# Optimization experiments

Measured on AMD Instinct MI355X. Metric: run time of the kernel, lower is better.

The kernel has to match this reference:

```python
import jax, jax.numpy as jnp
import numpy as np

B, T, C, H = 2, 2048, 1024, 16
D = C // H  # head dim = 64


def setup_inputs() -> dict:
    key = jax.random.key(0)
    ks = jax.random.split(key, 5)
    s = 0.02
    return {
        "x": jax.random.normal(ks[0], (B, T, C), dtype=jnp.float32),
        "W_attn": jax.random.normal(ks[1], (C, 3 * C), dtype=jnp.float32) * s,
        "b_attn": jax.random.normal(ks[2], (3 * C,), dtype=jnp.float32) * s,
        "W_proj": jax.random.normal(ks[3], (C, C), dtype=jnp.float32) * s,
        "b_proj": jax.random.normal(ks[4], (C,), dtype=jnp.float32) * s,
    }


def reference(x, W_attn, b_attn, W_proj, b_proj):
    Bb, Tt, Cc = x.shape
    kqv = x @ W_attn + b_attn                     # [B,T,3C]
    q, k, v = jnp.split(kqv, 3, axis=2)           # each [B,T,C]
    # reshape to heads: [B,H,T,D]
    q = q.reshape(Bb, Tt, H, D).transpose(0, 2, 1, 3)
    k = k.reshape(Bb, Tt, H, D).transpose(0, 2, 1, 3)
    v = v.reshape(Bb, Tt, H, D).transpose(0, 2, 1, 3)
    scale = 1.0 / jnp.sqrt(jnp.float32(D))
    att = jnp.einsum('bhqd,bhkd->bhqk', q, k) * scale  # [B,H,T,T]
    causal = jnp.tril(jnp.ones((Tt, Tt), dtype=bool))
    att = jnp.where(causal[None, None], att, -jnp.inf)
    att = jax.nn.softmax(att, axis=-1)
    y = jnp.einsum('bhqk,bhkd->bhqd', att, v)      # [B,H,T,D]
    y = y.transpose(0, 2, 1, 3).reshape(Bb, Tt, Cc)
    return y @ W_proj + b_proj
```

## Files before the change

### kernel.cpp

```cpp
#include <hip/hip_runtime.h>
#include <hip/hip_bf16.h>
#include <math.h>

typedef __attribute__((ext_vector_type(4))) float f32x4;
typedef __attribute__((ext_vector_type(8))) short short8;
typedef __attribute__((ext_vector_type(4))) short short4v;

__device__ __forceinline__ short f2bf(float f) {
    union { __hip_bfloat16 h; short s; } u;
    u.h = __float2bfloat16(f);
    return u.s;
}

__device__ __forceinline__ float bf2f(short s) {
    union { float f; unsigned u; } x;
    x.u = ((unsigned)(unsigned short)s) << 16;
    return x.f;
}

__device__ __forceinline__ f32x4 mfma16(short8 a, short8 b, f32x4 c) {
    return __builtin_amdgcn_mfma_f32_16x16x32_bf16(a, b, c, 0, 0, 0);
}

__global__ __launch_bounds__(256) void cvt_bf16(const float* __restrict__ in,
                                                short* __restrict__ out, int n) {
    int i = (blockIdx.x * 256 + threadIdx.x) * 8;
    if (i >= n) return;
    float4 a = *reinterpret_cast<const float4*>(in + i);
    float4 b = *reinterpret_cast<const float4*>(in + i + 4);
    short8 o;
    o[0] = f2bf(a.x); o[1] = f2bf(a.y); o[2] = f2bf(a.z); o[3] = f2bf(a.w);
    o[4] = f2bf(b.x); o[5] = f2bf(b.y); o[6] = f2bf(b.z); o[7] = f2bf(b.w);
    *reinterpret_cast<short8*>(out + i) = o;
}

__global__ __launch_bounds__(256) void transpose_w(const float* __restrict__ W,
                                                   short* __restrict__ Wt,
                                                   int K, int N) {
    __shared__ float tile[64][68];
    const int k0 = blockIdx.x * 64;
    const int n0 = blockIdx.y * 64;
    const int tid = threadIdx.x;
    #pragma unroll
    for (int i = 0; i < 4; ++i) {
        int c = tid + i * 256;
        int r = c >> 4;
        int col4 = (c & 15) * 4;
        float4 v = *reinterpret_cast<const float4*>(W + (size_t)(k0 + r) * N + n0 + col4);
        tile[r][col4 + 0] = v.x; tile[r][col4 + 1] = v.y;
        tile[r][col4 + 2] = v.z; tile[r][col4 + 3] = v.w;
    }
    __syncthreads();
    #pragma unroll
    for (int i = 0; i < 4; ++i) {
        int c = tid + i * 256;
        int r2 = c >> 4;
        int col4 = (c & 15) * 4;
        short4v o;
        #pragma unroll
        for (int j = 0; j < 4; ++j) o[j] = f2bf(tile[col4 + j][r2]);
        *reinterpret_cast<short4v*>(Wt + (size_t)(n0 + r2) * K + k0 + col4) = o;
    }
}

template<int MODE>
__global__ __launch_bounds__(256) void gemm_bt(const short* __restrict__ A,
                                               const short* __restrict__ Bt,
                                               const float* __restrict__ bias,
                                               void* __restrict__ C,
                                               short* __restrict__ vt,
                                               int M, int N, int K) {
    constexpr int BM = 128, BN = 128, BK = 64, LDP = BK + 8;
    __shared__ short As[BM * LDP];
    __shared__ short Bs[BN * LDP];
    const int tid = threadIdx.x;
    const int lane = tid & 63, wave = tid >> 6;
    const int bm = blockIdx.x * BM, bn = blockIdx.y * BN;
    const int wr = (wave >> 1) * 64, wc = (wave & 1) * 64;
    const int g = lane >> 4, l15 = lane & 15;

    f32x4 acc[4][4] = {};

    for (int k0 = 0; k0 < K; k0 += BK) {
        __syncthreads();
        #pragma unroll
        for (int i = 0; i < 4; ++i) {
            int c = tid + i * 256;
            int r = c >> 3;
            int col = (c & 7) * 8;
            *reinterpret_cast<short8*>(&As[r * LDP + col]) =
                *reinterpret_cast<const short8*>(A + (size_t)(bm + r) * K + k0 + col);
            *reinterpret_cast<short8*>(&Bs[r * LDP + col]) =
                *reinterpret_cast<const short8*>(Bt + (size_t)(bn + r) * K + k0 + col);
        }
        __syncthreads();
        #pragma unroll
        for (int kk = 0; kk < 2; ++kk) {
            short8 af[4], bfr[4];
            #pragma unroll
            for (int m = 0; m < 4; ++m)
                af[m] = *reinterpret_cast<const short8*>(&As[(wr + m * 16 + l15) * LDP + kk * 32 + g * 8]);
            #pragma unroll
            for (int n = 0; n < 4; ++n)
                bfr[n] = *reinterpret_cast<const short8*>(&Bs[(wc + n * 16 + l15) * LDP + kk * 32 + g * 8]);
            #pragma unroll
            for (int m = 0; m < 4; ++m)
                #pragma unroll
                for (int n = 0; n < 4; ++n)
                    acc[m][n] = mfma16(af[m], bfr[n], acc[m][n]);
        }
    }

    #pragma unroll
    for (int m = 0; m < 4; ++m)
        #pragma unroll
        for (int n = 0; n < 4; ++n) {
            int gc = bn + wc + n * 16 + l15;
            float bv = bias[gc];
            int gr0 = bm + wr + m * 16 + g * 4;
            if (MODE == 0) {
                #pragma unroll
                for (int r = 0; r < 4; ++r)
                    reinterpret_cast<float*>(C)[(size_t)(gr0 + r) * N + gc] = acc[m][n][r] + bv;
            } else {
                if (gc < 2048) {
                    float sc = (gc < 1024) ? 0.125f : 1.0f;
                    short* qkp = reinterpret_cast<short*>(C);
                    #pragma unroll
                    for (int r = 0; r < 4; ++r)
                        qkp[(size_t)(gr0 + r) * 2048 + gc] = f2bf((acc[m][n][r] + bv) * sc);
                } else {
                    int cv = gc - 2048;
                    int bb = gr0 >> 11;
                    int t0 = gr0 & 2047;
                    short4v o;
                    #pragma unroll
                    for (int r = 0; r < 4; ++r) o[r] = f2bf(acc[m][n][r] + bv);
                    *reinterpret_cast<short4v*>(&vt[((size_t)(bb << 10) + cv) * 2048 + t0]) = o;
                }
            }
        }
}


template<int NMAX, int KKMAX, bool MASK>
__device__ __forceinline__ void tile_step(const short* __restrict__ Kl,
                                          const short* __restrict__ Vl,
                                          short* Ps, int l15, int g,
                                          const short8 (&qf)[2][2],
                                          f32x4 (&oacc)[2][4],
                                          f32x4 (&lacc)[2],
                                          float (&mst)[2][4],
                                          int rowbase, int colbase,
                                          short8 ones) {
    f32x4 sacc[2][NMAX + 1];
    #pragma unroll
    for (int m = 0; m < 2; ++m)
        #pragma unroll
        for (int n = 0; n <= NMAX; ++n) sacc[m][n] = f32x4{0.f, 0.f, 0.f, 0.f};
    __builtin_amdgcn_s_setprio(1);
    #pragma unroll
    for (int kk = 0; kk < 2; ++kk)
        #pragma unroll
        for (int n = 0; n <= NMAX; ++n) {
            short8 kf = *reinterpret_cast<const short8*>(Kl + (size_t)n * 16 * 2048 + kk * 32);
            sacc[0][n] = mfma16(qf[0][kk], kf, sacc[0][n]);
            sacc[1][n] = mfma16(qf[1][kk], kf, sacc[1][n]);
        }
    __builtin_amdgcn_s_setprio(0);

    short8 vf[KKMAX + 1][4];
    #pragma unroll
    for (int kk = 0; kk <= KKMAX; ++kk)
        #pragma unroll
        for (int nd = 0; nd < 4; ++nd)
            vf[kk][nd] = *reinterpret_cast<const short8*>(Vl + (size_t)nd * 16 * 2048 + kk * 32);

    if (MASK) {
        #pragma unroll
        for (int m = 0; m < 2; ++m)
            #pragma unroll
            for (int n = 0; n <= NMAX; ++n)
                #pragma unroll
                for (int r = 0; r < 4; ++r) {
                    int row = rowbase + m * 16 + r;
                    int col = colbase + n * 16;
                    if (col > row) sacc[m][n][r] = -INFINITY;
                }
    }

    float rm[2][4];
    #pragma unroll
    for (int m = 0; m < 2; ++m)
        #pragma unroll
        for (int r = 0; r < 4; ++r) {
            float v = sacc[m][0][r];
            #pragma unroll
            for (int n = 1; n <= NMAX; ++n) v = fmaxf(v, sacc[m][n][r]);
            #pragma unroll
            for (int w = 1; w < 16; w <<= 1) v = fmaxf(v, __shfl_xor(v, w));
            rm[m][r] = v;
        }

    bool grow = false;
    #pragma unroll
    for (int m = 0; m < 2; ++m)
        #pragma unroll
        for (int r = 0; r < 4; ++r)
            grow = grow || (rm[m][r] > mst[m][r] + 8.0f);
    if (__any(grow)) {
        #pragma unroll
        for (int m = 0; m < 2; ++m)
            #pragma unroll
            for (int r = 0; r < 4; ++r) {
                float mn = fmaxf(mst[m][r], rm[m][r]);
                float corr = __expf(mst[m][r] - mn);
                mst[m][r] = mn;
                lacc[m][r] *= corr;
                #pragma unroll
                for (int nd = 0; nd < 4; ++nd) oacc[m][nd][r] *= corr;
            }
    }

    #pragma unroll
    for (int m = 0; m < 2; ++m)
        #pragma unroll
        for (int r = 0; r < 4; ++r) {
            #pragma unroll
            for (int n = 0; n <= NMAX; ++n) {
                float p = __expf(sacc[m][n][r] - mst[m][r]);
                Ps[(g * 4 + m * 16 + r) * 72 + n * 16 + l15] = f2bf(p);
            }
        }

    __builtin_amdgcn_s_setprio(1);
    #pragma unroll
    for (int kk = 0; kk <= KKMAX; ++kk) {
        short8 pa0 = *reinterpret_cast<const short8*>(&Ps[l15 * 72 + kk * 32 + g * 8]);
        short8 pa1 = *reinterpret_cast<const short8*>(&Ps[(16 + l15) * 72 + kk * 32 + g * 8]);
        #pragma unroll
        for (int nd = 0; nd < 4; ++nd) {
            oacc[0][nd] = mfma16(pa0, vf[kk][nd], oacc[0][nd]);
            oacc[1][nd] = mfma16(pa1, vf[kk][nd], oacc[1][nd]);
        }
        lacc[0] = mfma16(pa0, ones, lacc[0]);
        lacc[1] = mfma16(pa1, ones, lacc[1]);
    }
    __builtin_amdgcn_s_setprio(0);
}

__global__ __launch_bounds__(256) void attn_chunk(const short* __restrict__ qk,
                                                  const short* __restrict__ vt,
                                                  short* __restrict__ yatt,
                                                  short* __restrict__ part) {
    constexpr int T = 2048;
    __shared__ short PsAll[4][32 * 72];

    const int tid = threadIdx.x;
    const int wave = tid >> 6, lane = tid & 63;
    const int g = lane >> 4, l15 = lane & 15;
    short* Ps = PsAll[wave];

    const int bid = blockIdx.x;
    const int xcd = bid & 7;
    const int idx = bid >> 3;
    const int g4 = idx / 30;
    const int q = idx - g4 * 30;
    const int c = 119 - (q * 4 + wave);
    const int grp = xcd * 4 + g4;
    const int h = grp & 15, b = grp >> 4;
    int qt, ch;
    if (c < 24)      { qt = c; ch = 0; }
    else if (c < 72) { int t = c - 24; qt = 24 + (t >> 1); ch = t & 1; }
    else             { int t = c - 72; int q3 = t / 3; qt = 48 + q3; ch = t - q3 * 3; }

    const int nsteps = (qt >> 1) + 1;
    const int s0 = ch * 12;
    const int s1 = (s0 + 12 < nsteps) ? s0 + 12 : nsteps;
    const bool hasdiag = (s1 == nsteps);
    const int nfull = s1 - s0 - (hasdiag ? 1 : 0);

    const int qs = qt * 32;
    const size_t baseQ = (size_t)b * T * 2048 + (size_t)h * 64;
    const short* Kl = qk + baseQ + 1024 + (size_t)l15 * 2048 + g * 8;
    const short* Vl = vt + ((size_t)b * 1024 + (size_t)h * 64) * 2048 + (size_t)l15 * 2048 + g * 8;

    short8 ones;
    #pragma unroll
    for (int i = 0; i < 8; ++i) ones[i] = (short)0x3F80;

    short8 qf[2][2];
    #pragma unroll
    for (int m = 0; m < 2; ++m)
        #pragma unroll
        for (int kk = 0; kk < 2; ++kk)
            qf[m][kk] = *reinterpret_cast<const short8*>(
                qk + baseQ + (size_t)(qs + m * 16 + l15) * 2048 + kk * 32 + g * 8);

    f32x4 oacc[2][4] = {};
    f32x4 lacc[2] = {};
    float mst[2][4];
    #pragma unroll
    for (int m = 0; m < 2; ++m)
        #pragma unroll
        for (int r = 0; r < 4; ++r) mst[m][r] = -INFINITY;

    const int rowbase = qs + g * 4;
    int colbase = l15 + s0 * 64;
    const short* Klj = Kl + (size_t)s0 * 64 * 2048;
    const short* Vlj = Vl + s0 * 64;

    for (int j = 0; j < nfull; ++j) {
        tile_step<3, 1, false>(Klj, Vlj, Ps, l15, g, qf, oacc, lacc, mst, rowbase, colbase, ones);
        Klj += 64 * 2048;
        Vlj += 64;
        colbase += 64;
    }
    if (hasdiag) {
        if (qt & 1)
            tile_step<3, 1, true>(Klj, Vlj, Ps, l15, g, qf, oacc, lacc, mst, rowbase, colbase, ones);
        else
            tile_step<1, 0, true>(Klj, Vlj, Ps, l15, g, qf, oacc, lacc, mst, rowbase, colbase, ones);
    }

    if (qt < 24) {
        #pragma unroll
        for (int m = 0; m < 2; ++m)
            #pragma unroll
            for (int r = 0; r < 4; ++r) {
                float rl = 1.0f / lacc[m][r];
                int row = qs + m * 16 + g * 4 + r;
                #pragma unroll
                for (int nd = 0; nd < 4; ++nd) {
                    int col = nd * 16 + l15;
                    yatt[((size_t)b * T + row) * 1024 + h * 64 + col] = f2bf(oacc[m][nd][r] * rl);
                }
            }
    } else {
        const int p = grp * 96 + ((qt < 48) ? (qt - 24) * 2 + ch : 48 + (qt - 48) * 3 + ch);
        short* Pp = part + (size_t)p * 2112;
        #pragma unroll
        for (int m = 0; m < 2; ++m)
            #pragma unroll
            for (int r = 0; r < 4; ++r) {
                float rl = 1.0f / lacc[m][r];
                int rloc = m * 16 + g * 4 + r;
                #pragma unroll
                for (int nd = 0; nd < 4; ++nd)
                    Pp[rloc * 64 + nd * 16 + l15] = f2bf(oacc[m][nd][r] * rl);
            }
        if (l15 == 0) {
            float* Lp = reinterpret_cast<float*>(Pp + 2048);
            #pragma unroll
            for (int m = 0; m < 2; ++m)
                #pragma unroll
                for (int r = 0; r < 4; ++r)
                    Lp[m * 16 + g * 4 + r] = mst[m][r] + __logf(lacc[m][r]);
        }
    }
}

__global__ __launch_bounds__(64) void attn_merge(const short* __restrict__ part,
                                                 short* __restrict__ yatt) {
    const int bid = blockIdx.x;
    const int xcd = bid & 7;
    const int idx = bid >> 3;
    const int g4 = idx / 40;
    const int qt = 24 + (idx - g4 * 40);
    const int grp = xcd * 4 + g4;
    const int h = grp & 15, b = grp >> 4;
    const int nc = (qt < 48) ? 2 : 3;
    const int p0 = grp * 96 + ((qt < 48) ? (qt - 24) * 2 : 48 + (qt - 48) * 3);
    const int d = threadIdx.x & 63;

    const short* P0 = part + (size_t)p0 * 2112;
    #pragma unroll 4
    for (int r = 0; r < 32; ++r) {
        float lse[3], mx;
        lse[0] = reinterpret_cast<const float*>(P0 + 2048)[r];
        lse[1] = reinterpret_cast<const float*>(P0 + 2112 + 2048)[r];
        mx = fmaxf(lse[0], lse[1]);
        if (nc == 3) {
            lse[2] = reinterpret_cast<const float*>(P0 + 2 * 2112 + 2048)[r];
            mx = fmaxf(mx, lse[2]);
        }
        float w0 = __expf(lse[0] - mx);
        float w1 = __expf(lse[1] - mx);
        float wsum = w0 + w1;
        float acc = w0 * bf2f(P0[r * 64 + d]) + w1 * bf2f(P0[2112 + r * 64 + d]);
        if (nc == 3) {
            float w2 = __expf(lse[2] - mx);
            wsum += w2;
            acc += w2 * bf2f(P0[2 * 2112 + r * 64 + d]);
        }
        yatt[((size_t)b * 2048 + qt * 32 + r) * 1024 + h * 64 + d] = f2bf(acc / wsum);
    }
}

extern "C" void kernel_launch(void* const* d_in, const int* in_sizes, int n_in,
                              void* d_out, int out_size, void* d_ws, size_t ws_size,
                              hipStream_t stream) {
    constexpr int B = 2, T = 2048, C = 1024;
    constexpr int M = B * T;
    constexpr int N1 = 3 * C;
    constexpr int K = C;

    const float* x      = (const float*)d_in[0];
    const float* W_attn = (const float*)d_in[1];
    const float* b_attn = (const float*)d_in[2];
    const float* W_proj = (const float*)d_in[3];
    const float* b_proj = (const float*)d_in[4];
    float* out = (float*)d_out;

    char* ws = (char*)d_ws;
    short* x_bf    = (short*)(ws);
    short* Wt_attn = (short*)(ws + 8388608);
    short* Wt_proj = (short*)(ws + 14680064);
    short* qk      = (short*)(ws + 16777216);
    short* vt      = (short*)(ws + 33554432);
    short* yatt    = (short*)(ws + 41943040);
    short* part    = (short*)(ws);

    cvt_bf16<<<dim3(M * K / (256 * 8)), 256, 0, stream>>>(x, x_bf, M * K);
    transpose_w<<<dim3(K / 64, N1 / 64), 256, 0, stream>>>(W_attn, Wt_attn, K, N1);
    transpose_w<<<dim3(K / 64, C / 64), 256, 0, stream>>>(W_proj, Wt_proj, K, C);

    gemm_bt<1><<<dim3(M / 128, N1 / 128), 256, 0, stream>>>(x_bf, Wt_attn, b_attn, qk, vt, M, N1, K);
    attn_chunk<<<dim3(960), 256, 0, stream>>>(qk, vt, yatt, part);
    attn_merge<<<dim3(1280), 64, 0, stream>>>(part, yatt);
    gemm_bt<0><<<dim3(M / 128, C / 128), 256, 0, stream>>>(yatt, Wt_proj, b_proj, out, nullptr, M, C, C);
}
```

Measured before the change: 194.4 us.

## Share K/V tiles across waves via double-buffered LDS in chunked attention

Before, each wave owned its own 32-row query tile and read K and V straight from global memory. Now the four waves of a block cover one 128-row query tile and share 64-key K/V tiles staged through double-buffered LDS. The next tile is prefetched into registers while the current one is computed. The chunk and merge mapping is redone for 128-row tiles, and the merge kernel moves to 256-thread blocks. This cuts redundant global/L2 traffic for K and V, at the cost of block-wide barriers and coarser load balance across the causal triangle.

Result: slower. 221.4 us (+13.9%).

```diff
diff --git a/kernel.cpp b/kernel.cpp
--- a/kernel.cpp
+++ b/kernel.cpp
@@ -144,8 +144,7 @@
 
 
 template<int NMAX, int KKMAX, bool MASK>
-__device__ __forceinline__ void tile_step(const short* __restrict__ Kl,
-                                          const short* __restrict__ Vl,
+__device__ __forceinline__ void tile_step(const short* Kb, const short* Vb,
                                           short* Ps, int l15, int g,
                                           const short8 (&qf)[2][2],
                                           f32x4 (&oacc)[2][4],
@@ -163,7 +162,7 @@
     for (int kk = 0; kk < 2; ++kk)
         #pragma unroll
         for (int n = 0; n <= NMAX; ++n) {
-            short8 kf = *reinterpret_cast<const short8*>(Kl + (size_t)n * 16 * 2048 + kk * 32);
+            short8 kf = *reinterpret_cast<const short8*>(&Kb[(n * 16 + l15) * 72 + kk * 32 + g * 8]);
             sacc[0][n] = mfma16(qf[0][kk], kf, sacc[0][n]);
             sacc[1][n] = mfma16(qf[1][kk], kf, sacc[1][n]);
         }
@@ -174,7 +173,7 @@
     for (int kk = 0; kk <= KKMAX; ++kk)
         #pragma unroll
         for (int nd = 0; nd < 4; ++nd)
-            vf[kk][nd] = *reinterpret_cast<const short8*>(Vl + (size_t)nd * 16 * 2048 + kk * 32);
+            vf[kk][nd] = *reinterpret_cast<const short8*>(&Vb[(nd * 16 + l15) * 72 + kk * 32 + g * 8]);
 
     if (MASK) {
         #pragma unroll
@@ -254,6 +253,8 @@
                                                   short* __restrict__ yatt,
                                                   short* __restrict__ part) {
     constexpr int T = 2048;
+    __shared__ short Ks[2][64 * 72];
+    __shared__ short Vs[2][64 * 72];
     __shared__ short PsAll[4][32 * 72];
 
     const int tid = threadIdx.x;
@@ -264,26 +265,31 @@
     const int bid = blockIdx.x;
     const int xcd = bid & 7;
     const int idx = bid >> 3;
-    const int g4 = idx / 30;
-    const int q = idx - g4 * 30;
-    const int c = 119 - (q * 4 + wave);
+    const int g4 = idx & 3;
+    const int c = idx >> 2;
     const int grp = xcd * 4 + g4;
     const int h = grp & 15, b = grp >> 4;
+
     int qt, ch;
-    if (c < 24)      { qt = c; ch = 0; }
-    else if (c < 72) { int t = c - 24; qt = 24 + (t >> 1); ch = t & 1; }
-    else             { int t = c - 72; int q3 = t / 3; qt = 48 + q3; ch = t - q3 * 3; }
-
-    const int nsteps = (qt >> 1) + 1;
+    if (c < 8)       { qt = 12 + (c & 3); ch = c >> 2; }
+    else if (c < 14) { qt = 11 - (c - 8);  ch = 0; }
+    else if (c < 20) { qt = 11 - (c - 14); ch = 1; }
+    else if (c < 24) { qt = 12 + (c - 20); ch = 2; }
+    else             { qt = 5 - (c - 24);  ch = 0; }
+
+    const int nsteps = 2 * (qt + 1);
     const int s0 = ch * 12;
-    const int s1 = (s0 + 12 < nsteps) ? s0 + 12 : nsteps;
-    const bool hasdiag = (s1 == nsteps);
-    const int nfull = s1 - s0 - (hasdiag ? 1 : 0);
-
-    const int qs = qt * 32;
-    const size_t baseQ = (size_t)b * T * 2048 + (size_t)h * 64;
-    const short* Kl = qk + baseQ + 1024 + (size_t)l15 * 2048 + g * 8;
-    const short* Vl = vt + ((size_t)b * 1024 + (size_t)h * 64) * 2048 + (size_t)l15 * 2048 + g * 8;
+    const int schunk = (nsteps - s0 < 12) ? (nsteps - s0) : 12;
+    const bool hasdiag = (s0 + schunk == nsteps);
+    const int qs = qt * 128;
+    const int q0w = qs + wave * 32;
+
+    const size_t baseQ  = (size_t)b * T * 2048 + (size_t)h * 64;
+    const short* kg0 = qk + baseQ + 1024;
+    const short* vg0 = vt + ((size_t)b * 1024 + (size_t)h * 64) * 2048;
+
+    const int sr0 = tid >> 3;
+    const int sc0 = (tid & 7) * 8;
 
     short8 ones;
     #pragma unroll
@@ -295,7 +301,7 @@
         #pragma unroll
         for (int kk = 0; kk < 2; ++kk)
             qf[m][kk] = *reinterpret_cast<const short8*>(
-                qk + baseQ + (size_t)(qs + m * 16 + l15) * 2048 + kk * 32 + g * 8);
+                qk + baseQ + (size_t)(q0w + m * 16 + l15) * 2048 + kk * 32 + g * 8);
 
     f32x4 oacc[2][4] = {};
     f32x4 lacc[2] = {};
@@ -305,31 +311,70 @@
         #pragma unroll
         for (int r = 0; r < 4; ++r) mst[m][r] = -INFINITY;
 
-    const int rowbase = qs + g * 4;
-    int colbase = l15 + s0 * 64;
-    const short* Klj = Kl + (size_t)s0 * 64 * 2048;
-    const short* Vlj = Vl + s0 * 64;
-
-    for (int j = 0; j < nfull; ++j) {
-        tile_step<3, 1, false>(Klj, Vlj, Ps, l15, g, qf, oacc, lacc, mst, rowbase, colbase, ones);
-        Klj += 64 * 2048;
-        Vlj += 64;
-        colbase += 64;
-    }
-    if (hasdiag) {
-        if (qt & 1)
-            tile_step<3, 1, true>(Klj, Vlj, Ps, l15, g, qf, oacc, lacc, mst, rowbase, colbase, ones);
-        else
-            tile_step<1, 0, true>(Klj, Vlj, Ps, l15, g, qf, oacc, lacc, mst, rowbase, colbase, ones);
-    }
-
-    if (qt < 24) {
+    {
+        const short* kg = kg0 + (size_t)(s0 * 64) * 2048;
+        const short* vg = vg0 + s0 * 64;
+        #pragma unroll
+        for (int i = 0; i < 2; ++i) {
+            int row = sr0 + i * 32;
+            *reinterpret_cast<short8*>(&Ks[0][row * 72 + sc0]) =
+                *reinterpret_cast<const short8*>(&kg[(size_t)row * 2048 + sc0]);
+            *reinterpret_cast<short8*>(&Vs[0][row * 72 + sc0]) =
+                *reinterpret_cast<const short8*>(&vg[(size_t)row * 2048 + sc0]);
+        }
+        __syncthreads();
+    }
+
+    const int rowbase = q0w + g * 4;
+    int cur = 0;
+
+    for (int j = 0; j < schunk; ++j) {
+        const int tileidx = s0 + j;
+        const bool more = (j + 1 < schunk);
+
+        short8 kr0, kr1, vr0, vr1;
+        if (more) {
+            const short* kg = kg0 + (size_t)((tileidx + 1) * 64) * 2048;
+            const short* vg = vg0 + (tileidx + 1) * 64;
+            kr0 = *reinterpret_cast<const short8*>(&kg[(size_t)sr0 * 2048 + sc0]);
+            kr1 = *reinterpret_cast<const short8*>(&kg[(size_t)(sr0 + 32) * 2048 + sc0]);
+            vr0 = *reinterpret_cast<const short8*>(&vg[(size_t)sr0 * 2048 + sc0]);
+            vr1 = *reinterpret_cast<const short8*>(&vg[(size_t)(sr0 + 32) * 2048 + sc0]);
+        }
+
+        const short* Kb = Ks[cur];
+        const short* Vb = Vs[cur];
+        const int colbase = l15 + tileidx * 64;
+
+        if (!hasdiag || j < schunk - 2) {
+            tile_step<3, 1, false>(Kb, Vb, Ps, l15, g, qf, oacc, lacc, mst, rowbase, colbase, ones);
+        } else if (j == schunk - 2) {
+            if (wave == 0)      tile_step<1, 0, true >(Kb, Vb, Ps, l15, g, qf, oacc, lacc, mst, rowbase, colbase, ones);
+            else if (wave == 1) tile_step<3, 1, true >(Kb, Vb, Ps, l15, g, qf, oacc, lacc, mst, rowbase, colbase, ones);
+            else                tile_step<3, 1, false>(Kb, Vb, Ps, l15, g, qf, oacc, lacc, mst, rowbase, colbase, ones);
+        } else {
+            if (wave == 2)      tile_step<1, 0, true >(Kb, Vb, Ps, l15, g, qf, oacc, lacc, mst, rowbase, colbase, ones);
+            else if (wave == 3) tile_step<3, 1, true >(Kb, Vb, Ps, l15, g, qf, oacc, lacc, mst, rowbase, colbase, ones);
+        }
+
+        if (more) {
+            int nxt = cur ^ 1;
+            *reinterpret_cast<short8*>(&Ks[nxt][sr0 * 72 + sc0]) = kr0;
+            *reinterpret_cast<short8*>(&Ks[nxt][(sr0 + 32) * 72 + sc0]) = kr1;
+            *reinterpret_cast<short8*>(&Vs[nxt][sr0 * 72 + sc0]) = vr0;
+            *reinterpret_cast<short8*>(&Vs[nxt][(sr0 + 32) * 72 + sc0]) = vr1;
+            __syncthreads();
+            cur = nxt;
+        }
+    }
+
+    if (qt < 6) {
         #pragma unroll
         for (int m = 0; m < 2; ++m)
             #pragma unroll
             for (int r = 0; r < 4; ++r) {
                 float rl = 1.0f / lacc[m][r];
-                int row = qs + m * 16 + g * 4 + r;
+                int row = q0w + m * 16 + g * 4 + r;
                 #pragma unroll
                 for (int nd = 0; nd < 4; ++nd) {
                     int col = nd * 16 + l15;
@@ -337,63 +382,65 @@
                 }
             }
     } else {
-        const int p = grp * 96 + ((qt < 48) ? (qt - 24) * 2 + ch : 48 + (qt - 48) * 3 + ch);
-        short* Pp = part + (size_t)p * 2112;
+        const int slot = (qt < 12) ? ((qt - 6) * 2 + ch) : (12 + (qt - 12) * 3 + ch);
+        short* Pp = part + (size_t)(grp * 24 + slot) * 8448;
         #pragma unroll
         for (int m = 0; m < 2; ++m)
             #pragma unroll
             for (int r = 0; r < 4; ++r) {
                 float rl = 1.0f / lacc[m][r];
-                int rloc = m * 16 + g * 4 + r;
+                int rloc = wave * 32 + m * 16 + g * 4 + r;
                 #pragma unroll
                 for (int nd = 0; nd < 4; ++nd)
                     Pp[rloc * 64 + nd * 16 + l15] = f2bf(oacc[m][nd][r] * rl);
             }
         if (l15 == 0) {
-            float* Lp = reinterpret_cast<float*>(Pp + 2048);
+            float* Lp = reinterpret_cast<float*>(Pp + 8192);
             #pragma unroll
             for (int m = 0; m < 2; ++m)
                 #pragma unroll
                 for (int r = 0; r < 4; ++r)
-                    Lp[m * 16 + g * 4 + r] = mst[m][r] + __logf(lacc[m][r]);
-        }
-    }
-}
-
-__global__ __launch_bounds__(64) void attn_merge(const short* __restrict__ part,
-                                                 short* __restrict__ yatt) {
+                    Lp[wave * 32 + m * 16 + g * 4 + r] = mst[m][r] + __logf(lacc[m][r]);
+        }
+    }
+}
+
+__global__ __launch_bounds__(256) void attn_merge(const short* __restrict__ part,
+                                                  short* __restrict__ yatt) {
     const int bid = blockIdx.x;
     const int xcd = bid & 7;
     const int idx = bid >> 3;
-    const int g4 = idx / 40;
-    const int qt = 24 + (idx - g4 * 40);
+    const int g4 = idx / 10;
+    const int qt = 6 + (idx - g4 * 10);
     const int grp = xcd * 4 + g4;
     const int h = grp & 15, b = grp >> 4;
-    const int nc = (qt < 48) ? 2 : 3;
-    const int p0 = grp * 96 + ((qt < 48) ? (qt - 24) * 2 : 48 + (qt - 48) * 3);
+    const int nc = (qt < 12) ? 2 : 3;
+    const int p0 = grp * 24 + ((qt < 12) ? (qt - 6) * 2 : 12 + (qt - 12) * 3);
+    const int wave = threadIdx.x >> 6;
     const int d = threadIdx.x & 63;
 
-    const short* P0 = part + (size_t)p0 * 2112;
+    const short* P0 = part + (size_t)p0 * 8448;
     #pragma unroll 4
-    for (int r = 0; r < 32; ++r) {
+    for (int rr = 0; rr < 32; ++rr) {
+        int r = wave * 32 + rr;
         float lse[3], mx;
-        lse[0] = reinterpret_cast<const float*>(P0 + 2048)[r];
-        lse[1] = reinterpret_cast<const float*>(P0 + 2112 + 2048)[r];
+        lse[0] = reinterpret_cast<const float*>(P0 + 8192)[r];
+        lse[1] = reinterpret_cast<const float*>(P0 + 8448 + 8192)[r];
         mx = fmaxf(lse[0], lse[1]);
         if (nc == 3) {
-            lse[2] = reinterpret_cast<const float*>(P0 + 2 * 2112 + 2048)[r];
+            lse[2] = reinterpret_cast<const float*>(P0 + 2 * 8448 + 8192)[r];
             mx = fmaxf(mx, lse[2]);
         }
         float w0 = __expf(lse[0] - mx);
         float w1 = __expf(lse[1] - mx);
         float wsum = w0 + w1;
-        float acc = w0 * bf2f(P0[r * 64 + d]) + w1 * bf2f(P0[2112 + r * 64 + d]);
+        float acc = w0 * bf2f(P0[r * 64 + d]) + w1 * bf2f(P0[8448 + r * 64 + d]);
         if (nc == 3) {
             float w2 = __expf(lse[2] - mx);
             wsum += w2;
-            acc += w2 * bf2f(P0[2 * 2112 + r * 64 + d]);
-        }
-        yatt[((size_t)b * 2048 + qt * 32 + r) * 1024 + h * 64 + d] = f2bf(acc / wsum);
+            acc += w2 * bf2f(P0[2 * 8448 + r * 64 + d]);
+        }
+        yatt[((size_t)b * 2048 + qt * 128 + r) * 1024 + h * 64 + d] = f2bf(acc / wsum);
     }
 }
 
@@ -427,6 +474,6 @@
 
     gemm_bt<1><<<dim3(M / 128, N1 / 128), 256, 0, stream>>>(x_bf, Wt_attn, b_attn, qk, vt, M, N1, K);
     attn_chunk<<<dim3(960), 256, 0, stream>>>(qk, vt, yatt, part);
-    attn_merge<<<dim3(1280), 64, 0, stream>>>(part, yatt);
+    attn_merge<<<dim3(320), 256, 0, stream>>>(part, yatt);
     gemm_bt<0><<<dim3(M / 128, C / 128), 256, 0, stream>>>(yatt, Wt_proj, b_proj, out, nullptr, M, C, C);
 }
```

## Store Q, K, V in head-major contiguous layouts for attention loads

Applied to the files above, without the earlier changes.

The QKV GEMM epilogue now writes Q and K as [B,H,T,64] and V as 64x64 tiles transposed per head and key block, replacing the interleaved [B,T,2048] QK buffer and the [B,C,T] V transpose. The attention kernel's K and V fragment loads then hit a contiguous 8KB region per key tile instead of rows strided by 4KB, which should improve cache and TLB locality. The cost is scattered 2-byte stores for Q and K in the GEMM epilogue, which may be less coalesced.

After: 194.9 us. About the same (+0.3%).

```diff
diff --git a/kernel.cpp b/kernel.cpp
--- a/kernel.cpp
+++ b/kernel.cpp
@@ -68,7 +68,9 @@
                                                const short* __restrict__ Bt,
                                                const float* __restrict__ bias,
                                                void* __restrict__ C,
-                                               short* __restrict__ vt,
+                                               short* __restrict__ qp,
+                                               short* __restrict__ kp,
+                                               short* __restrict__ vp,
                                                int M, int N, int K) {
     constexpr int BM = 128, BN = 128, BK = 64, LDP = BK + 8;
     __shared__ short As[BM * LDP];
@@ -123,20 +125,27 @@
                 for (int r = 0; r < 4; ++r)
                     reinterpret_cast<float*>(C)[(size_t)(gr0 + r) * N + gc] = acc[m][n][r] + bv;
             } else {
-                if (gc < 2048) {
-                    float sc = (gc < 1024) ? 0.125f : 1.0f;
-                    short* qkp = reinterpret_cast<short*>(C);
+                const int bb = gr0 >> 11;
+                const int t0 = gr0 & 2047;
+                if (gc < 1024) {
+                    int hh = gc >> 6, d = gc & 63;
+                    size_t base = (((size_t)bb * 16 + hh) * 2048 + t0) * 64 + d;
                     #pragma unroll
                     for (int r = 0; r < 4; ++r)
-                        qkp[(size_t)(gr0 + r) * 2048 + gc] = f2bf((acc[m][n][r] + bv) * sc);
+                        qp[base + (size_t)r * 64] = f2bf((acc[m][n][r] + bv) * 0.125f);
+                } else if (gc < 2048) {
+                    int hh = (gc - 1024) >> 6, d = gc & 63;
+                    size_t base = (((size_t)bb * 16 + hh) * 2048 + t0) * 64 + d;
+                    #pragma unroll
+                    for (int r = 0; r < 4; ++r)
+                        kp[base + (size_t)r * 64] = f2bf(acc[m][n][r] + bv);
                 } else {
-                    int cv = gc - 2048;
-                    int bb = gr0 >> 11;
-                    int t0 = gr0 & 2047;
+                    int hh = (gc - 2048) >> 6, d = gc & 63;
                     short4v o;
                     #pragma unroll
                     for (int r = 0; r < 4; ++r) o[r] = f2bf(acc[m][n][r] + bv);
-                    *reinterpret_cast<short4v*>(&vt[((size_t)(bb << 10) + cv) * 2048 + t0]) = o;
+                    size_t base = ((((size_t)bb * 16 + hh) * 32 + (t0 >> 6)) * 64 + d) * 64 + (t0 & 63);
+                    *reinterpret_cast<short4v*>(&vp[base]) = o;
                 }
             }
         }
@@ -163,7 +172,7 @@
     for (int kk = 0; kk < 2; ++kk)
         #pragma unroll
         for (int n = 0; n <= NMAX; ++n) {
-            short8 kf = *reinterpret_cast<const short8*>(Kl + (size_t)n * 16 * 2048 + kk * 32);
+            short8 kf = *reinterpret_cast<const short8*>(Kl + n * 1024 + kk * 32);
             sacc[0][n] = mfma16(qf[0][kk], kf, sacc[0][n]);
             sacc[1][n] = mfma16(qf[1][kk], kf, sacc[1][n]);
         }
@@ -174,7 +183,7 @@
     for (int kk = 0; kk <= KKMAX; ++kk)
         #pragma unroll
         for (int nd = 0; nd < 4; ++nd)
-            vf[kk][nd] = *reinterpret_cast<const short8*>(Vl + (size_t)nd * 16 * 2048 + kk * 32);
+            vf[kk][nd] = *reinterpret_cast<const short8*>(Vl + nd * 1024 + kk * 32);
 
     if (MASK) {
         #pragma unroll
@@ -249,8 +258,9 @@
     __builtin_amdgcn_s_setprio(0);
 }
 
-__global__ __launch_bounds__(256) void attn_chunk(const short* __restrict__ qk,
-                                                  const short* __restrict__ vt,
+__global__ __launch_bounds__(256) void attn_chunk(const short* __restrict__ qp,
+                                                  const short* __restrict__ kp,
+                                                  const short* __restrict__ vp,
                                                   short* __restrict__ yatt,
                                                   short* __restrict__ part) {
     constexpr int T = 2048;
@@ -281,9 +291,10 @@
     const int nfull = s1 - s0 - (hasdiag ? 1 : 0);
 
     const int qs = qt * 32;
-    const size_t baseQ = (size_t)b * T * 2048 + (size_t)h * 64;
-    const short* Kl = qk + baseQ + 1024 + (size_t)l15 * 2048 + g * 8;
-    const short* Vl = vt + ((size_t)b * 1024 + (size_t)h * 64) * 2048 + (size_t)l15 * 2048 + g * 8;
+    const size_t bh = (size_t)(b * 16 + h);
+    const short* qp_bh = qp + bh * (2048 * 64);
+    const short* Kl = kp + bh * (2048 * 64) + l15 * 64 + g * 8;
+    const short* Vl = vp + bh * (32 * 4096) + l15 * 64 + g * 8;
 
     short8 ones;
     #pragma unroll
@@ -295,7 +306,7 @@
         #pragma unroll
         for (int kk = 0; kk < 2; ++kk)
             qf[m][kk] = *reinterpret_cast<const short8*>(
-                qk + baseQ + (size_t)(qs + m * 16 + l15) * 2048 + kk * 32 + g * 8);
+                qp_bh + (size_t)(qs + m * 16 + l15) * 64 + kk * 32 + g * 8);
 
     f32x4 oacc[2][4] = {};
     f32x4 lacc[2] = {};
@@ -307,13 +318,13 @@
 
     const int rowbase = qs + g * 4;
     int colbase = l15 + s0 * 64;
-    const short* Klj = Kl + (size_t)s0 * 64 * 2048;
-    const short* Vlj = Vl + s0 * 64;
+    const short* Klj = Kl + (size_t)s0 * 4096;
+    const short* Vlj = Vl + (size_t)s0 * 4096;
 
     for (int j = 0; j < nfull; ++j) {
         tile_step<3, 1, false>(Klj, Vlj, Ps, l15, g, qf, oacc, lacc, mst, rowbase, colbase, ones);
-        Klj += 64 * 2048;
-        Vlj += 64;
+        Klj += 4096;
+        Vlj += 4096;
         colbase += 64;
     }
     if (hasdiag) {
@@ -416,8 +427,9 @@
     short* x_bf    = (short*)(ws);
     short* Wt_attn = (short*)(ws + 8388608);
     short* Wt_proj = (short*)(ws + 14680064);
-    short* qk      = (short*)(ws + 16777216);
-    short* vt      = (short*)(ws + 33554432);
+    short* qp      = (short*)(ws + 16777216);
+    short* kp      = (short*)(ws + 25165824);
+    short* vp      = (short*)(ws + 33554432);
     short* yatt    = (short*)(ws + 41943040);
     short* part    = (short*)(ws);
 
@@ -425,8 +437,8 @@
     transpose_w<<<dim3(K / 64, N1 / 64), 256, 0, stream>>>(W_attn, Wt_attn, K, N1);
     transpose_w<<<dim3(K / 64, C / 64), 256, 0, stream>>>(W_proj, Wt_proj, K, C);
 
-    gemm_bt<1><<<dim3(M / 128, N1 / 128), 256, 0, stream>>>(x_bf, Wt_attn, b_attn, qk, vt, M, N1, K);
-    attn_chunk<<<dim3(960), 256, 0, stream>>>(qk, vt, yatt, part);
+    gemm_bt<1><<<dim3(M / 128, N1 / 128), 256, 0, stream>>>(x_bf, Wt_attn, b_attn, nullptr, qp, kp, vp, M, N1, K);
+    attn_chunk<<<dim3(960), 256, 0, stream>>>(qp, kp, vp, yatt, part);
     attn_merge<<<dim3(1280), 64, 0, stream>>>(part, yatt);
-    gemm_bt<0><<<dim3(M / 128, C / 128), 256, 0, stream>>>(yatt, Wt_proj, b_proj, out, nullptr, M, C, C);
-}
+    gemm_bt<0><<<dim3(M / 128, C / 128), 256, 0, stream>>>(yatt, Wt_proj, b_proj, out, nullptr, nullptr, nullptr, M, C, C);
+}
```
